# Kernel optimization log

Hardware: AMD Instinct MI355X
Metric: run time of the kernel (lower is better)

Reference implementation:

```python
import jax, jax.numpy as jnp
import numpy as np

HEAD_NUM = 16
D_MODEL = 1024
D_K = D_MODEL // HEAD_NUM


def setup_inputs() -> dict:
    key = jax.random.key(0)
    ks = jax.random.split(key, 11)
    B, S = 2, 2048
    scale = 1.0 / np.sqrt(D_MODEL)
    inp = {
        'query': jax.random.normal(ks[0], (B, S, D_MODEL), jnp.float32),
        'key': jax.random.normal(ks[1], (B, S, D_MODEL), jnp.float32),
        'value': jax.random.normal(ks[2], (B, S, D_MODEL), jnp.float32),
        'W1': jax.random.normal(ks[3], (D_MODEL, D_MODEL), jnp.float32) * scale,
        'b1': jax.random.normal(ks[4], (D_MODEL,), jnp.float32) * 0.02,
        'W2': jax.random.normal(ks[5], (D_MODEL, D_MODEL), jnp.float32) * scale,
        'b2': jax.random.normal(ks[6], (D_MODEL,), jnp.float32) * 0.02,
        'W3': jax.random.normal(ks[7], (D_MODEL, D_MODEL), jnp.float32) * scale,
        'b3': jax.random.normal(ks[8], (D_MODEL,), jnp.float32) * 0.02,
        'W4': jax.random.normal(ks[9], (D_MODEL, D_MODEL), jnp.float32) * scale,
        'b4': jax.random.normal(ks[10], (D_MODEL,), jnp.float32) * 0.02,
    }
    return inp


def reference(query, key, value, W1, b1, W2, b2, W3, b3, W4, b4):
    B, S, _ = query.shape
    # linear projections (torch Linear: x @ W^T + b)
    q = query @ W1.T + b1
    k = key @ W2.T + b2
    v = value @ W3.T + b3
    # [B, H, S, d_k]
    q = q.reshape(B, S, HEAD_NUM, D_K).transpose(0, 2, 1, 3)
    k = k.reshape(B, S, HEAD_NUM, D_K).transpose(0, 2, 1, 3)
    v = v.reshape(B, S, HEAD_NUM, D_K).transpose(0, 2, 1, 3)
    # scaled dot-product attention
    scores = jnp.einsum('bhqd,bhkd->bhqk', q, k) / np.sqrt(D_K).astype(jnp.float32)
    attn = jax.nn.softmax(scores, axis=-1)
    out = jnp.einsum('bhqk,bhkd->bhqd', attn, v)
    # merge heads -> [B, S, d_model]
    out = out.transpose(0, 2, 1, 3).reshape(B, S, D_MODEL)
    result = out @ W4.T + b4
    return result
```

## Files before the change

### kernel.cpp

```cpp
#include <hip/hip_runtime.h>
#include <hip/hip_bf16.h>
#include <stdint.h>

typedef unsigned short u16;
typedef unsigned int   u32;
typedef __attribute__((ext_vector_type(4))) float f32x4;
typedef __attribute__((ext_vector_type(8))) short bf16x8;

__device__ __forceinline__ u16 f2bf(float x){
  u32 u = __float_as_uint(x);
  return (u16)((u + 0x7fffu + ((u >> 16) & 1u)) >> 16);
}

__device__ __forceinline__ u32 pkbf(float a, float b){
  __hip_bfloat162 t = __float22bfloat162_rn(make_float2(a, b));
  u32 r; __builtin_memcpy(&r, &t, 4); return r;
}

__device__ __forceinline__ float fexp2(float x){
  float r; asm("v_exp_f32 %0, %1" : "=v"(r) : "v"(x)); return r;
}

__device__ __forceinline__ void pl16swap(u32 &d, u32 &s){
  asm("v_permlane16_swap_b32 %0, %1" : "+v"(d), "+v"(s));
}

__device__ __forceinline__ bf16x8 mk8(u32 a, u32 b, u32 c, u32 d){
  union { u32 w[4]; bf16x8 v; } t; t.w[0]=a; t.w[1]=b; t.w[2]=c; t.w[3]=d; return t.v;
}

__device__ __forceinline__ void async_cp16(const void* g, void* l){
  __builtin_amdgcn_global_load_lds((const __attribute__((address_space(1))) void*)g,
                                   (__attribute__((address_space(3))) void*)l, 16, 0, 0);
}

__device__ __forceinline__ void conv_body(const float* __restrict__ x,
                                          u16* __restrict__ hi, int i){
  float4 v = *(const float4*)(x + i);
  ushort4 hv; hv.x = f2bf(v.x); hv.y = f2bf(v.y); hv.z = f2bf(v.z); hv.w = f2bf(v.w);
  *(ushort4*)(hi + i) = hv;
}

__global__ __launch_bounds__(256) void conv_all(
    const float* __restrict__ q, const float* __restrict__ k, const float* __restrict__ v,
    const float* __restrict__ w1, const float* __restrict__ w2,
    const float* __restrict__ w3, const float* __restrict__ w4,
    u16* qh, u16* kh, u16* vh, u16* w1h, u16* w2h, u16* w3h, u16* w4h)
{
  const int o = blockIdx.x;
  const float* x; u16* y; int blk;
  if (o < 12288){
    const int z = o >> 12;
    blk = o & 4095;
    x = (z == 0) ? q : (z == 1) ? k : v;
    y = (z == 0) ? qh : (z == 1) ? kh : vh;
  } else {
    const int o2 = o - 12288;
    const int z = o2 >> 10;
    blk = o2 & 1023;
    x = (z == 0) ? w1 : (z == 1) ? w2 : (z == 2) ? w3 : w4;
    y = (z == 0) ? w1h : (z == 1) ? w2h : (z == 2) ? w3h : w4h;
  }
  conv_body(x, y, (blk * 256 + threadIdx.x) * 4);
}

template<int OUT>
__device__ __forceinline__ void gemm_plain(
    const u16* __restrict__ A, const u16* __restrict__ B,
    const float* __restrict__ bias, void* __restrict__ outp, float scale, int m0, int n0)
{
  __shared__ u16 lA[4096], lB[4096];
  const int tid  = threadIdx.x;
  const int lane = tid & 63, wid = tid >> 6;
  const int li = lane & 15, g = lane >> 4;
  const int wr = wid >> 1, wc = wid & 1;

  const u16* pA = A + (size_t)m0 * 1024;
  const u16* pB = B + (size_t)n0 * 1024;

  const int c0i = tid,        r0 = c0i >> 2, ch0 = c0i & 3;
  const int c1i = 256 + tid,  r1 = c1i >> 2, ch1 = c1i & 3;
  const size_t g0 = (size_t)r0 * 1024 + (size_t)((ch0 ^ (r0 & 3)) * 8);
  const size_t g1 = (size_t)r1 * 1024 + (size_t)((ch1 ^ (r1 & 3)) * 8);
  const int l0 = (wid * 64) * 8;
  const int l1 = (256 + wid * 64) * 8;

  f32x4 acc[4][4];
  #pragma unroll
  for (int i = 0; i < 4; i++)
    #pragma unroll
    for (int j = 0; j < 4; j++) acc[i][j] = (f32x4){0.f, 0.f, 0.f, 0.f};

  for (int k0 = 0; k0 < 1024; k0 += 32){
    __syncthreads();
    async_cp16(pA + g0 + k0, lA + l0);
    async_cp16(pA + g1 + k0, lA + l1);
    async_cp16(pB + g0 + k0, lB + l0);
    async_cp16(pB + g1 + k0, lB + l1);
    __syncthreads();

    bf16x8 af[4], bf4[4];
    #pragma unroll
    for (int f = 0; f < 4; f++){
      int ar = wr * 64 + f * 16 + li;
      af[f] = *(const bf16x8*)&lA[ar * 32 + (g ^ (ar & 3)) * 8];
      int br = wc * 64 + f * 16 + li;
      bf4[f] = *(const bf16x8*)&lB[br * 32 + (g ^ (br & 3)) * 8];
    }
    __builtin_amdgcn_s_setprio(1);
    #pragma unroll
    for (int fm = 0; fm < 4; fm++)
      #pragma unroll
      for (int fn = 0; fn < 4; fn++)
        acc[fm][fn] = __builtin_amdgcn_mfma_f32_16x16x32_bf16(af[fm], bf4[fn], acc[fm][fn], 0, 0, 0);
    __builtin_amdgcn_s_setprio(0);
  }

  float bv[4];
  #pragma unroll
  for (int fn = 0; fn < 4; fn++) bv[fn] = bias[n0 + wc * 64 + fn * 16 + li];

  #pragma unroll
  for (int fm = 0; fm < 4; fm++){
    const int mb = m0 + wr * 64 + fm * 16 + g * 4;
    #pragma unroll
    for (int fn = 0; fn < 4; fn++){
      const int n = n0 + wc * 64 + fn * 16 + li;
      #pragma unroll
      for (int r = 0; r < 4; r++){
        float v = acc[fm][fn][r] + bv[fn];
        if (OUT == 0) ((u16*)outp)[(size_t)(mb + r) * 1024 + n] = f2bf(v * scale);
        else          ((float*)outp)[(size_t)(mb + r) * 1024 + n] = v;
      }
    }
  }
}

__global__ __launch_bounds__(256, 2) void proj_kernel(
    const u16* qh, const u16* kh, const u16* vh,
    const u16* w1h, const u16* w2h, const u16* w3h,
    const float* b1, const float* b2, const float* b3,
    u16* Qb, u16* Kb, u16* Vb)
{
  const int o = blockIdx.x;
  const int swz = (o & 7) * 96 + (o >> 3);
  const int x = swz & 7, y = (swz >> 3) & 31, z = swz >> 8;
  const u16 *A, *B; const float* bs; u16* out; float sc;
  if (z == 0){ A = qh; B = w1h; bs = b1; out = Qb; sc = 0.18033688011112042f; }
  else if (z == 1){ A = kh; B = w2h; bs = b2; out = Kb; sc = 1.0f; }
  else { A = vh; B = w3h; bs = b3; out = Vb; sc = 1.0f; }
  gemm_plain<0>(A, B, bs, out, sc, y * 128, x * 128);
}

__global__ __launch_bounds__(256, 2) void fin_kernel(
    const u16* __restrict__ A, const u16* __restrict__ B,
    const float* __restrict__ bias, float* __restrict__ out)
{
  const int o = blockIdx.x;
  const int swz = (o & 7) * 32 + (o >> 3);
  const int x = swz & 7, y = swz >> 3;
  gemm_plain<1>(A, B, bias, out, 1.0f, y * 128, x * 128);
}

__global__ __launch_bounds__(256) void transpose_v(const u16* __restrict__ Vb, u16* __restrict__ VbT){
  __shared__ u16 T[64][72];
  const int t = threadIdx.x;
  const int kt = blockIdx.x, h = blockIdx.y, b = blockIdx.z;
  const int r = t >> 2, c0 = (t & 3) * 16;
  const u16* src = Vb + (size_t)(b * 2048 + kt * 64 + r) * 1024 + h * 64 + c0;
  *(bf16x8*)&T[r][c0]     = *(const bf16x8*)(src);
  *(bf16x8*)&T[r][c0 + 8] = *(const bf16x8*)(src + 8);
  __syncthreads();
  const int d = t >> 2, kc = (t & 3) * 16;
  bf16x8 o0, o1;
  #pragma unroll
  for (int j = 0; j < 8; j++){ o0[j] = (short)T[kc + j][d]; o1[j] = (short)T[kc + 8 + j][d]; }
  u16* dst = VbT + ((size_t)(b * 16 + h) * 64 + d) * 2048 + kt * 64 + kc;
  *(bf16x8*)dst       = o0;
  *(bf16x8*)(dst + 8) = o1;
}

__global__ __launch_bounds__(256) void attn_kernel(
    const u16* __restrict__ Qb, const u16* __restrict__ Kb, const u16* __restrict__ VbT,
    u16* __restrict__ AOh)
{
  __shared__ u16 KT[2][4096];
  __shared__ u16 VT[2][4096];
  char* Kc = (char*)KT; char* Vc = (char*)VT;

  const int tid = threadIdx.x;
  const int lane = tid & 63, wid = tid >> 6;
  const int li = lane & 15, g = lane >> 4;

  const int o = blockIdx.x;
  const int swz = (o & 7) * 128 + (o >> 3);
  const int qt = swz & 31, h = (swz >> 5) & 15, b = swz >> 9;

  const int r0 = tid >> 3, ch = tid & 7;
  const int cswz8 = (ch ^ (r0 & 7)) * 8;
  const u16* gK = Kb  + (size_t)(b * 2048 + r0) * 1024 + h * 64 + cswz8;
  const u16* gV = VbT + ((size_t)(b * 16 + h) * 64 + r0) * 2048 + cswz8;
  const int ldsB = wid * 1024;

  const int kb0 = li * 128 + ((g ^ (li & 7)) << 4);
  const int gsw = ((((g & 1) << 1) | ((g >> 1) & 1)) ^ 2);
  const int vb0 = li * 128 + ((gsw ^ (li & 7)) << 4);

  const u16* qp = Qb + (size_t)(b * 2048 + qt * 64 + wid * 16 + li) * 1024 + h * 64 + g * 8;
  bf16x8 qf[2];
  qf[0] = *(const bf16x8*)(qp);
  qf[1] = *(const bf16x8*)(qp + 32);

  f32x4 O[4];
  #pragma unroll
  for (int df = 0; df < 4; df++) O[df] = (f32x4){0.f, 0.f, 0.f, 0.f};
  f32x4 Lacc = (f32x4){0.f, 0.f, 0.f, 0.f};
  const f32x4 NEGC = (f32x4){-32.f, -32.f, -32.f, -32.f};
  const u32 one2 = 0x3f803f80u;
  const bf16x8 ones = mk8(one2, one2, one2, one2);

  #pragma unroll
  for (int s = 0; s < 2; s++){
    async_cp16(gK + s * 32768, Kc + ldsB + s * 4096);
    async_cp16(gV + s * 65536, Vc + ldsB + s * 4096);
  }

  int cur = 0;
  for (int t = 0; t < 32; t++){
    if (t < 31){
      const int kn = (t + 1) * 64;
      const int nb = (cur ^ 1) * 8192;
      #pragma unroll
      for (int s = 0; s < 2; s++){
        async_cp16(gK + (size_t)kn * 1024 + s * 32768, Kc + nb + ldsB + s * 4096);
        async_cp16(gV + kn + s * 65536,                Vc + nb + ldsB + s * 4096);
      }
      asm volatile("s_waitcnt vmcnt(4)" ::: "memory");
    } else {
      asm volatile("s_waitcnt vmcnt(0)" ::: "memory");
    }
    __builtin_amdgcn_sched_barrier(0);
    __builtin_amdgcn_s_barrier();
    __builtin_amdgcn_sched_barrier(0);

    const char* Kb_ = Kc + cur * 8192;
    const char* Vb_ = Vc + cur * 8192;

    f32x4 sc_[4];
    __builtin_amdgcn_s_setprio(1);
    #pragma unroll
    for (int fn = 0; fn < 4; fn++){
      bf16x8 kf0 = *(const bf16x8*)(Kb_ + fn * 2048 + kb0);
      bf16x8 kf1 = *(const bf16x8*)(Kb_ + fn * 2048 + (kb0 ^ 64));
      f32x4 z = __builtin_amdgcn_mfma_f32_16x16x32_bf16(kf0, qf[0], NEGC, 0, 0, 0);
      sc_[fn] = __builtin_amdgcn_mfma_f32_16x16x32_bf16(kf1, qf[1], z, 0, 0, 0);
    }
    __builtin_amdgcn_s_setprio(0);

    float p[4][4];
    #pragma unroll
    for (int fn = 0; fn < 4; fn++)
      #pragma unroll
      for (int r = 0; r < 4; r++)
        p[fn][r] = fexp2(sc_[fn][r]);

    bf16x8 pa[2];
    #pragma unroll
    for (int ks = 0; ks < 2; ks++){
      u32 a0 = pkbf(p[2 * ks][0],     p[2 * ks][1]);
      u32 a1 = pkbf(p[2 * ks][2],     p[2 * ks][3]);
      u32 b0 = pkbf(p[2 * ks + 1][0], p[2 * ks + 1][1]);
      u32 b1 = pkbf(p[2 * ks + 1][2], p[2 * ks + 1][3]);
      pl16swap(b0, a0);
      pl16swap(b1, a1);
      pa[ks] = mk8(b0, b1, a0, a1);
    }

    __builtin_amdgcn_s_setprio(1);
    #pragma unroll
    for (int ks = 0; ks < 2; ks++){
      Lacc = __builtin_amdgcn_mfma_f32_16x16x32_bf16(ones, pa[ks], Lacc, 0, 0, 0);
      #pragma unroll
      for (int df = 0; df < 4; df++){
        bf16x8 vf = *(const bf16x8*)(Vb_ + df * 2048 + (vb0 ^ (ks << 6)));
        O[df] = __builtin_amdgcn_mfma_f32_16x16x32_bf16(vf, pa[ks], O[df], 0, 0, 0);
      }
    }
    __builtin_amdgcn_s_setprio(0);

    __builtin_amdgcn_sched_barrier(0);
    __builtin_amdgcn_s_barrier();
    cur ^= 1;
  }

  const float inv = 1.0f / Lacc[0];
  const int rowb = b * 2048 + qt * 64 + wid * 16;
  #pragma unroll
  for (int df = 0; df < 4; df++){
    ushort4 hv;
    #pragma unroll
    for (int r = 0; r < 4; r++)
      ((u16*)&hv)[r] = f2bf(O[df][r] * inv);
    size_t idx = (size_t)(rowb + li) * 1024 + h * 64 + df * 16 + g * 4;
    *(ushort4*)(AOh + idx) = hv;
  }
}

extern "C" void kernel_launch(void* const* d_in, const int* in_sizes, int n_in,
                              void* d_out, int out_size, void* d_ws, size_t ws_size,
                              hipStream_t stream)
{
  (void)in_sizes; (void)n_in; (void)out_size; (void)ws_size;
  const float* query = (const float*)d_in[0];
  const float* key_  = (const float*)d_in[1];
  const float* value = (const float*)d_in[2];
  const float* W1 = (const float*)d_in[3];
  const float* b1 = (const float*)d_in[4];
  const float* W2 = (const float*)d_in[5];
  const float* b2 = (const float*)d_in[6];
  const float* W3 = (const float*)d_in[7];
  const float* b3 = (const float*)d_in[8];
  const float* W4 = (const float*)d_in[9];
  const float* b4 = (const float*)d_in[10];

  char* w = (char*)d_ws;
  const size_t MB = (size_t)1 << 20;
  u16* qh  = (u16*)(w +  0 * MB);
  u16* kh  = (u16*)(w +  8 * MB);
  u16* vh  = (u16*)(w + 16 * MB);
  u16* w1h = (u16*)(w + 24 * MB);
  u16* w2h = (u16*)(w + 26 * MB);
  u16* w3h = (u16*)(w + 28 * MB);
  u16* w4h = (u16*)(w + 30 * MB);
  u16* Qb  = (u16*)(w + 32 * MB);
  u16* Kb  = (u16*)(w + 40 * MB);
  u16* Vb  = (u16*)(w + 48 * MB);
  u16* VbT = (u16*)(w + 56 * MB);
  u16* AOh = (u16*)(w + 64 * MB);

  conv_all<<<16384, 256, 0, stream>>>(query, key_, value, W1, W2, W3, W4,
                                      qh, kh, vh, w1h, w2h, w3h, w4h);

  proj_kernel<<<768, 256, 0, stream>>>(qh, kh, vh, w1h, w2h, w3h, b1, b2, b3, Qb, Kb, Vb);
  transpose_v<<<dim3(32, 16, 2), 256, 0, stream>>>(Vb, VbT);
  attn_kernel<<<1024, 256, 0, stream>>>(Qb, Kb, VbT, AOh);
  fin_kernel<<<256, 256, 0, stream>>>(AOh, w4h, b4, (float*)d_out);
}
```

Measured before the change: 136.9 us.

## Process two 16-row query subtiles per wave to reuse K/V tiles

Each wave in the attention kernel now handles 32 query rows (two 16-row subtiles) instead of 16, so each block covers 128 queries and the grid halves to 512 blocks. Each K and V fragment read from LDS is reused for two MFMA streams, halving global and LDS traffic for K/V per query. The cost is more accumulator registers, which may lower occupancy, and fewer blocks (512 on 256 CUs) to balance across the device.

```diff
diff --git a/kernel.cpp b/kernel.cpp
--- a/kernel.cpp
+++ b/kernel.cpp
@@ -193,8 +193,8 @@
   const int li = lane & 15, g = lane >> 4;
 
   const int o = blockIdx.x;
-  const int swz = (o & 7) * 128 + (o >> 3);
-  const int qt = swz & 31, h = (swz >> 5) & 15, b = swz >> 9;
+  const int swz = (o & 7) * 64 + (o >> 3);
+  const int qt = swz & 15, h = (swz >> 4) & 15, b = swz >> 8;
 
   const int r0 = tid >> 3, ch = tid & 7;
   const int cswz8 = (ch ^ (r0 & 7)) * 8;
@@ -206,15 +206,21 @@
   const int gsw = ((((g & 1) << 1) | ((g >> 1) & 1)) ^ 2);
   const int vb0 = li * 128 + ((gsw ^ (li & 7)) << 4);
 
-  const u16* qp = Qb + (size_t)(b * 2048 + qt * 64 + wid * 16 + li) * 1024 + h * 64 + g * 8;
-  bf16x8 qf[2];
-  qf[0] = *(const bf16x8*)(qp);
-  qf[1] = *(const bf16x8*)(qp + 32);
-
-  f32x4 O[4];
-  #pragma unroll
-  for (int df = 0; df < 4; df++) O[df] = (f32x4){0.f, 0.f, 0.f, 0.f};
-  f32x4 Lacc = (f32x4){0.f, 0.f, 0.f, 0.f};
+  const u16* qp = Qb + (size_t)(b * 2048 + qt * 128 + wid * 32 + li) * 1024 + h * 64 + g * 8;
+  bf16x8 qf[2][2];
+  qf[0][0] = *(const bf16x8*)(qp);
+  qf[0][1] = *(const bf16x8*)(qp + 32);
+  qf[1][0] = *(const bf16x8*)(qp + 16 * 1024);
+  qf[1][1] = *(const bf16x8*)(qp + 16 * 1024 + 32);
+
+  f32x4 O[2][4];
+  #pragma unroll
+  for (int st = 0; st < 2; st++)
+    #pragma unroll
+    for (int df = 0; df < 4; df++) O[st][df] = (f32x4){0.f, 0.f, 0.f, 0.f};
+  f32x4 Lacc[2];
+  Lacc[0] = (f32x4){0.f, 0.f, 0.f, 0.f};
+  Lacc[1] = (f32x4){0.f, 0.f, 0.f, 0.f};
   const f32x4 NEGC = (f32x4){-32.f, -32.f, -32.f, -32.f};
   const u32 one2 = 0x3f803f80u;
   const bf16x8 ones = mk8(one2, one2, one2, one2);
@@ -246,44 +252,52 @@
     const char* Kb_ = Kc + cur * 8192;
     const char* Vb_ = Vc + cur * 8192;
 
-    f32x4 sc_[4];
+    f32x4 sc_[2][4];
     __builtin_amdgcn_s_setprio(1);
     #pragma unroll
     for (int fn = 0; fn < 4; fn++){
       bf16x8 kf0 = *(const bf16x8*)(Kb_ + fn * 2048 + kb0);
       bf16x8 kf1 = *(const bf16x8*)(Kb_ + fn * 2048 + (kb0 ^ 64));
-      f32x4 z = __builtin_amdgcn_mfma_f32_16x16x32_bf16(kf0, qf[0], NEGC, 0, 0, 0);
-      sc_[fn] = __builtin_amdgcn_mfma_f32_16x16x32_bf16(kf1, qf[1], z, 0, 0, 0);
+      #pragma unroll
+      for (int st = 0; st < 2; st++){
+        f32x4 z = __builtin_amdgcn_mfma_f32_16x16x32_bf16(kf0, qf[st][0], NEGC, 0, 0, 0);
+        sc_[st][fn] = __builtin_amdgcn_mfma_f32_16x16x32_bf16(kf1, qf[st][1], z, 0, 0, 0);
+      }
     }
     __builtin_amdgcn_s_setprio(0);
 
-    float p[4][4];
-    #pragma unroll
-    for (int fn = 0; fn < 4; fn++)
-      #pragma unroll
-      for (int r = 0; r < 4; r++)
-        p[fn][r] = fexp2(sc_[fn][r]);
-
-    bf16x8 pa[2];
+    bf16x8 pa[2][2];
+    #pragma unroll
+    for (int st = 0; st < 2; st++){
+      float p[4][4];
+      #pragma unroll
+      for (int fn = 0; fn < 4; fn++)
+        #pragma unroll
+        for (int r = 0; r < 4; r++)
+          p[fn][r] = fexp2(sc_[st][fn][r]);
+
+      #pragma unroll
+      for (int ks = 0; ks < 2; ks++){
+        u32 a0 = pkbf(p[2 * ks][0],     p[2 * ks][1]);
+        u32 a1 = pkbf(p[2 * ks][2],     p[2 * ks][3]);
+        u32 b0 = pkbf(p[2 * ks + 1][0], p[2 * ks + 1][1]);
+        u32 b1 = pkbf(p[2 * ks + 1][2], p[2 * ks + 1][3]);
+        pl16swap(b0, a0);
+        pl16swap(b1, a1);
+        pa[st][ks] = mk8(b0, b1, a0, a1);
+      }
+    }
+
+    __builtin_amdgcn_s_setprio(1);
     #pragma unroll
     for (int ks = 0; ks < 2; ks++){
-      u32 a0 = pkbf(p[2 * ks][0],     p[2 * ks][1]);
-      u32 a1 = pkbf(p[2 * ks][2],     p[2 * ks][3]);
-      u32 b0 = pkbf(p[2 * ks + 1][0], p[2 * ks + 1][1]);
-      u32 b1 = pkbf(p[2 * ks + 1][2], p[2 * ks + 1][3]);
-      pl16swap(b0, a0);
-      pl16swap(b1, a1);
-      pa[ks] = mk8(b0, b1, a0, a1);
-    }
-
-    __builtin_amdgcn_s_setprio(1);
-    #pragma unroll
-    for (int ks = 0; ks < 2; ks++){
-      Lacc = __builtin_amdgcn_mfma_f32_16x16x32_bf16(ones, pa[ks], Lacc, 0, 0, 0);
+      Lacc[0] = __builtin_amdgcn_mfma_f32_16x16x32_bf16(ones, pa[0][ks], Lacc[0], 0, 0, 0);
+      Lacc[1] = __builtin_amdgcn_mfma_f32_16x16x32_bf16(ones, pa[1][ks], Lacc[1], 0, 0, 0);
       #pragma unroll
       for (int df = 0; df < 4; df++){
         bf16x8 vf = *(const bf16x8*)(Vb_ + df * 2048 + (vb0 ^ (ks << 6)));
-        O[df] = __builtin_amdgcn_mfma_f32_16x16x32_bf16(vf, pa[ks], O[df], 0, 0, 0);
+        O[0][df] = __builtin_amdgcn_mfma_f32_16x16x32_bf16(vf, pa[0][ks], O[0][df], 0, 0, 0);
+        O[1][df] = __builtin_amdgcn_mfma_f32_16x16x32_bf16(vf, pa[1][ks], O[1][df], 0, 0, 0);
       }
     }
     __builtin_amdgcn_s_setprio(0);
@@ -293,16 +307,19 @@
     cur ^= 1;
   }
 
-  const float inv = 1.0f / Lacc[0];
-  const int rowb = b * 2048 + qt * 64 + wid * 16;
-  #pragma unroll
-  for (int df = 0; df < 4; df++){
-    ushort4 hv;
-    #pragma unroll
-    for (int r = 0; r < 4; r++)
-      ((u16*)&hv)[r] = f2bf(O[df][r] * inv);
-    size_t idx = (size_t)(rowb + li) * 1024 + h * 64 + df * 16 + g * 4;
-    *(ushort4*)(AOh + idx) = hv;
+  const int rowb = b * 2048 + qt * 128 + wid * 32;
+  #pragma unroll
+  for (int st = 0; st < 2; st++){
+    const float inv = 1.0f / Lacc[st][0];
+    #pragma unroll
+    for (int df = 0; df < 4; df++){
+      ushort4 hv;
+      #pragma unroll
+      for (int r = 0; r < 4; r++)
+        ((u16*)&hv)[r] = f2bf(O[st][df][r] * inv);
+      size_t idx = (size_t)(rowb + st * 16 + li) * 1024 + h * 64 + df * 16 + g * 4;
+      *(ushort4*)(AOh + idx) = hv;
+    }
   }
 }
 
@@ -343,6 +360,6 @@
 
   proj_kernel<<<768, 256, 0, stream>>>(qh, kh, vh, w1h, w2h, w3h, b1, b2, b3, Qb, Kb, Vb);
   transpose_v<<<dim3(32, 16, 2), 256, 0, stream>>>(Vb, VbT);
-  attn_kernel<<<1024, 256, 0, stream>>>(Qb, Kb, VbT, AOh);
+  attn_kernel<<<512, 256, 0, stream>>>(Qb, Kb, VbT, AOh);
   fin_kernel<<<256, 256, 0, stream>>>(AOh, w4h, b4, (float*)d_out);
 }
```

Result: no change. 135.7 us (-0.9%).
